# Kernel tuning notes

Hardware: AMD Instinct MI355X
Metric: run time of the kernel (lower is better)

## Reference

```python
import jax, jax.numpy as jnp
import numpy as np

N = 100000          # nodes
E = 3200000         # edges
F_IN = 128          # num_node_features
C = 32              # num_candidate_node_types


def _gcn_conv(x, src, dst, W, b, n_nodes):
    """PyG GCNConv: add self loops, symmetric deg^-1/2 normalization, then linear."""
    h = x @ W  # [N, out]
    # degree on A + I (edge weight 1), counted on target nodes
    deg = jnp.zeros((n_nodes,), h.dtype).at[dst].add(1.0) + 1.0
    dinv = jax.lax.rsqrt(deg)  # deg >= 1 so safe
    norm = dinv[src] * dinv[dst]            # [E]
    msg = h[src] * norm[:, None]            # gather + scale, [E, out]
    out = jax.ops.segment_sum(msg, dst, num_segments=n_nodes)
    out = out + h * (dinv * dinv)[:, None]  # self-loop contribution
    return out + b


def _relu6(x):
    return jnp.clip(x, 0.0, 6.0)


def setup_inputs() -> dict:
    key = jax.random.key(0)
    ks = jax.random.split(key, 16)
    def lin(k, fan_in, fan_out):
        lim = 1.0 / np.sqrt(fan_in)
        kw, kb = jax.random.split(k)
        W = jax.random.uniform(kw, (fan_in, fan_out), jnp.float32, -lim, lim)
        b = jax.random.uniform(kb, (fan_out,), jnp.float32, -lim, lim)
        return W, b
    W1, b1 = lin(ks[0], F_IN, 16)
    W2, b2 = lin(ks[1], 16, 24)
    W3, b3 = lin(ks[2], 24, 32)
    Ws1, bs1 = lin(ks[3], 32, 16)
    Ws2, bs2 = lin(ks[4], 16, C)
    We1, be1 = lin(ks[5], 32, 24)
    We2, be2 = lin(ks[6], 24, C)
    x = jax.random.normal(ks[7], (N, F_IN), jnp.float32)
    edge_index = jax.random.randint(ks[8], (2, E), 0, N, jnp.int64)
    candidate_set = jax.random.randint(ks[9], (C,), 0, C, jnp.int64)
    return dict(x=x, edge_index=edge_index, candidate_set=candidate_set,
                W1=W1, b1=b1, W2=W2, b2=b2, W3=W3, b3=b3,
                Ws1=Ws1, bs1=bs1, Ws2=Ws2, bs2=bs2,
                We1=We1, be1=be1, We2=We2, be2=be2)


def reference(x, edge_index, candidate_set,
              W1, b1, W2, b2, W3, b3,
              Ws1, bs1, Ws2, bs2, We1, be1, We2, be2):
    src, dst = edge_index[0], edge_index[1]
    h = _gcn_conv(x, src, dst, W1, b1, N)   # [N, 16] (no activation in source)
    h = _gcn_conv(h, src, dst, W2, b2, N)   # [N, 24]
    h = _gcn_conv(h, src, dst, W3, b3, N)   # [N, 32]
    # start-node head: Linear -> ReLU6 -> Linear -> Softmax, then Categorical sample
    s_logits = _relu6(h @ Ws1 + bs1) @ Ws2 + bs2         # [N, C]
    k1, k2 = jax.random.split(jax.random.key(42))
    start_node = jax.random.categorical(k1, s_logits, axis=-1)  # [N] ints in [0, C)
    # gather rows at sampled indices and append (vectorized form of the source's cat)
    combined = jnp.concatenate([h, h[start_node]], axis=0)      # [2N, 32]
    e_logits = _relu6(combined @ We1 + be1) @ We2 + be2          # [2N, C]
    end_node = jax.random.categorical(k2, e_logits, axis=-1)    # [2N]
    return start_node, end_node
```

## Files before the change

### kernel.cpp

```cpp
#include <hip/hip_runtime.h>
#include <hip/hip_bf16.h>
#include <math.h>

#define TPB 256
#define BSHIFT 8
#define BRANGE (1 << BSHIFT)
#define CHUNK 8192
#define MAXB 512

__host__ __device__ inline void tf2x32(unsigned ks0, unsigned ks1,
                                       unsigned x0, unsigned x1,
                                       unsigned& o0, unsigned& o1) {
  const unsigned ks2 = ks0 ^ ks1 ^ 0x1BD11BDAu;
  unsigned v0 = x0 + ks0, v1 = x1 + ks1;
#define TF_RND(r) { v0 += v1; v1 = (v1 << (r)) | (v1 >> (32 - (r))); v1 ^= v0; }
  TF_RND(13) TF_RND(15) TF_RND(26) TF_RND(6)
  v0 += ks1; v1 += ks2 + 1u;
  TF_RND(17) TF_RND(29) TF_RND(16) TF_RND(24)
  v0 += ks2; v1 += ks0 + 2u;
  TF_RND(13) TF_RND(15) TF_RND(26) TF_RND(6)
  v0 += ks0; v1 += ks1 + 3u;
  TF_RND(17) TF_RND(29) TF_RND(16) TF_RND(24)
  v0 += ks1; v1 += ks2 + 4u;
  TF_RND(13) TF_RND(15) TF_RND(26) TF_RND(6)
  v0 += ks2; v1 += ks0 + 5u;
#undef TF_RND
  o0 = v0; o1 = v1;
}

__device__ __forceinline__ unsigned bits32(unsigned k0, unsigned k1, unsigned idx) {
  unsigned o0, o1;
  tf2x32(k0, k1, 0u, idx, o0, o1);
  return o0 ^ o1;
}

__device__ __forceinline__ float bits_to_u(unsigned bits) {
  float f = __uint_as_float((bits >> 9) | 0x3f800000u) - 1.0f;
  return (f > 0.0f) ? f : 1.17549435e-38f;
}

__device__ __forceinline__ float gumbel_exact(unsigned k0, unsigned k1, unsigned idx) {
  float u = bits_to_u(bits32(k0, k1, idx));
  float w = (float)(-log((double)u));
  return (float)(-log((double)w));
}

__device__ __forceinline__ float gumbel_fast(unsigned k0, unsigned k1, unsigned idx) {
  float u = bits_to_u(bits32(k0, k1, idx));
  float w = -logf(u);
  return -logf(w);
}

__global__ void hist_kernel(const int* __restrict__ dst, int* __restrict__ histT,
                            int E, int nblk, int nbuckets) {
  __shared__ int hist[MAXB];
  for (int i = threadIdx.x; i < nbuckets; i += TPB) hist[i] = 0;
  __syncthreads();
  int beg = blockIdx.x * CHUNK;
  int end = min(beg + CHUNK, E);
  for (int e = beg + threadIdx.x; e < end; e += TPB)
    atomicAdd(&hist[dst[e] >> BSHIFT], 1);
  __syncthreads();
  for (int i = threadIdx.x; i < nbuckets; i += TPB)
    histT[(size_t)i * nblk + blockIdx.x] = hist[i];
}

__global__ void colscan_kernel(int* __restrict__ histT, int* __restrict__ btot, int nblk) {
  __shared__ int sh[MAXB];
  int b = blockIdx.x;
  int t = threadIdx.x;
  sh[t] = (t < nblk) ? histT[(size_t)b * nblk + t] : 0;
  __syncthreads();
  for (int ofs = 1; ofs < MAXB; ofs <<= 1) {
    int v = (t >= ofs) ? sh[t - ofs] : 0;
    __syncthreads();
    sh[t] += v;
    __syncthreads();
  }
  if (t < nblk) histT[(size_t)b * nblk + t] = (t == 0) ? 0 : sh[t - 1];
  if (t == MAXB - 1) btot[b] = sh[MAXB - 1];
}

__global__ void bucketscan_kernel(const int* __restrict__ btot, int* __restrict__ bbase,
                                  int nbuckets, int E) {
  __shared__ int sh[MAXB];
  int t = threadIdx.x;
  sh[t] = (t < nbuckets) ? btot[t] : 0;
  __syncthreads();
  for (int ofs = 1; ofs < MAXB; ofs <<= 1) {
    int v = (t >= ofs) ? sh[t - ofs] : 0;
    __syncthreads();
    sh[t] += v;
    __syncthreads();
  }
  if (t < nbuckets) bbase[t] = (t == 0) ? 0 : sh[t - 1];
  if (t == 0) bbase[nbuckets] = E;
}

__global__ void place_kernel(const int* __restrict__ src, const int* __restrict__ dst,
                             const int* __restrict__ histT, const int* __restrict__ bbase,
                             unsigned* __restrict__ packed, int E, int nblk, int nbuckets) {
  __shared__ int cur[MAXB];
  for (int i = threadIdx.x; i < nbuckets; i += TPB)
    cur[i] = histT[(size_t)i * nblk + blockIdx.x] + bbase[i];
  __syncthreads();
  int beg = blockIdx.x * CHUNK;
  int end = min(beg + CHUNK, E);
  for (int e = beg + threadIdx.x; e < end; e += TPB) {
    int s = src[e], d = dst[e];
    int b = d >> BSHIFT;
    int pos = atomicAdd(&cur[b], 1);
    packed[pos] = (unsigned)s | ((unsigned)(d & (BRANGE - 1)) << 20);
  }
}

__global__ void bucket_place_kernel(const int* __restrict__ bbase,
                                    const unsigned* __restrict__ packed,
                                    int* __restrict__ csr_src, int* __restrict__ rowptr,
                                    float* __restrict__ dinv, float* __restrict__ dinv2,
                                    int N, int nbuckets) {
  __shared__ int cnt[BRANGE];
  __shared__ int sh[BRANGE];
  __shared__ int cur[BRANGE];
  int b = blockIdx.x;
  int base = b << BSHIFT;
  int range_n = min(BRANGE, N - base);
  int t = threadIdx.x;
  cnt[t] = 0;
  __syncthreads();
  int beg = bbase[b], end = bbase[b + 1];
  for (int e = beg + t; e < end; e += TPB)
    atomicAdd(&cnt[packed[e] >> 20], 1);
  __syncthreads();
  sh[t] = cnt[t];
  __syncthreads();
  for (int ofs = 1; ofs < BRANGE; ofs <<= 1) {
    int v = (t >= ofs) ? sh[t - ofs] : 0;
    __syncthreads();
    sh[t] += v;
    __syncthreads();
  }
  int excl = (t == 0) ? 0 : sh[t - 1];
  cur[t] = beg + excl;
  if (t < range_n) {
    rowptr[base + t] = beg + excl;
    float d = (float)(cnt[t] + 1);
    float di = 1.0f / sqrtf(d);
    dinv[base + t] = di;
    dinv2[base + t] = di * di;
  }
  if (b == nbuckets - 1 && t == 0) rowptr[N] = end;
  __syncthreads();
  for (int e = beg + t; e < end; e += TPB) {
    unsigned p = packed[e];
    int dstoff = (int)(p >> 20);
    int s = (int)(p & 0xFFFFFu);
    int pos = atomicAdd(&cur[dstoff], 1);
    csr_src[pos] = s;
  }
}

template <int K, int J, int LDO, int TJ>
__global__ void matmul_tile_kernel(const float* __restrict__ A, const float* __restrict__ W,
                                   float* __restrict__ out, int N) {
  static_assert(J == TJ * 4, "each thread owns 4 outputs");
  static_assert(K % 4 == 0, "K must be multiple of 4");
  int t = blockIdx.x * blockDim.x + threadIdx.x;
  int n = t / TJ, jb = t % TJ;
  if (n >= N) return;
  const float* a = A + (size_t)n * K;
  const int j0 = jb * 4;
  double a0 = 0.0, a1 = 0.0, a2 = 0.0, a3 = 0.0;
  for (int k = 0; k < K; k += 4) {
    float4 av = *(const float4*)&a[k];
    float4 w0 = *(const float4*)&W[(k + 0) * J + j0];
    float4 w1 = *(const float4*)&W[(k + 1) * J + j0];
    float4 w2 = *(const float4*)&W[(k + 2) * J + j0];
    float4 w3 = *(const float4*)&W[(k + 3) * J + j0];
    a0 += (double)av.x * (double)w0.x; a1 += (double)av.x * (double)w0.y;
    a2 += (double)av.x * (double)w0.z; a3 += (double)av.x * (double)w0.w;
    a0 += (double)av.y * (double)w1.x; a1 += (double)av.y * (double)w1.y;
    a2 += (double)av.y * (double)w1.z; a3 += (double)av.y * (double)w1.w;
    a0 += (double)av.z * (double)w2.x; a1 += (double)av.z * (double)w2.y;
    a2 += (double)av.z * (double)w2.z; a3 += (double)av.z * (double)w2.w;
    a0 += (double)av.w * (double)w3.x; a1 += (double)av.w * (double)w3.y;
    a2 += (double)av.w * (double)w3.z; a3 += (double)av.w * (double)w3.w;
  }
  float4 o;
  o.x = (float)a0; o.y = (float)a1; o.z = (float)a2; o.w = (float)a3;
  *(float4*)&out[(size_t)n * LDO + j0] = o;
}

template <int J>
__global__ void gather_shfl_kernel(const int* __restrict__ rowptr,
                                   const int* __restrict__ csr_src,
                                   const float* __restrict__ dinv,
                                   const float* __restrict__ h,
                                   const float* __restrict__ dinv2,
                                   const float* __restrict__ b,
                                   float* __restrict__ out, int N) {
  int t = blockIdx.x * blockDim.x + threadIdx.x;
  int n = t / J, j = t % J;
  if (n >= N) return;
  int beg = rowptr[n], end = rowptr[n + 1];
  float dn = dinv[n];
  double acc = 0.0;
  for (int i = beg; i < end; i += J) {
    int m = end - i; if (m > J) m = J;
    int idx = i + j; if (idx >= end) idx = end - 1;
    int   sj = csr_src[idx];
    float wj = dinv[sj];
    int k = 0;
    for (; k + 8 <= m; k += 8) {
      int s0 = __shfl(sj, k + 0, J), s1 = __shfl(sj, k + 1, J);
      int s2 = __shfl(sj, k + 2, J), s3 = __shfl(sj, k + 3, J);
      int s4 = __shfl(sj, k + 4, J), s5 = __shfl(sj, k + 5, J);
      int s6 = __shfl(sj, k + 6, J), s7 = __shfl(sj, k + 7, J);
      float w0 = __shfl(wj, k + 0, J) * dn, w1 = __shfl(wj, k + 1, J) * dn;
      float w2 = __shfl(wj, k + 2, J) * dn, w3 = __shfl(wj, k + 3, J) * dn;
      float w4 = __shfl(wj, k + 4, J) * dn, w5 = __shfl(wj, k + 5, J) * dn;
      float w6 = __shfl(wj, k + 6, J) * dn, w7 = __shfl(wj, k + 7, J) * dn;
      float g0 = h[(size_t)s0 * J + j], g1 = h[(size_t)s1 * J + j];
      float g2 = h[(size_t)s2 * J + j], g3 = h[(size_t)s3 * J + j];
      float g4 = h[(size_t)s4 * J + j], g5 = h[(size_t)s5 * J + j];
      float g6 = h[(size_t)s6 * J + j], g7 = h[(size_t)s7 * J + j];
      acc += (double)g0 * (double)w0;
      acc += (double)g1 * (double)w1;
      acc += (double)g2 * (double)w2;
      acc += (double)g3 * (double)w3;
      acc += (double)g4 * (double)w4;
      acc += (double)g5 * (double)w5;
      acc += (double)g6 * (double)w6;
      acc += (double)g7 * (double)w7;
    }
    for (; k < m; ++k) {
      int   s = __shfl(sj, k, J);
      float w = __shfl(wj, k, J) * dn;
      acc += (double)h[(size_t)s * J + j] * (double)w;
    }
  }
  acc += (double)h[(size_t)n * J + j] * (double)dinv2[n];
  out[(size_t)n * J + j] = (float)acc + b[j];
}

template <int JA, int W, int LDH>
__global__ void gather_shfl2_kernel(const int* __restrict__ rowptr,
                                    const int* __restrict__ csr_src,
                                    const float* __restrict__ dinv,
                                    const float* __restrict__ h,
                                    const float* __restrict__ dinv2,
                                    const float* __restrict__ b,
                                    float* __restrict__ out, int N) {
  int t = blockIdx.x * blockDim.x + threadIdx.x;
  int n = t / W, j = t % W;
  if (n >= N) return;
  const int NJ = JA / 2;
  int jj = (j < NJ) ? j : (NJ - 1);
  int beg = rowptr[n], end = rowptr[n + 1];
  float dn = dinv[n];
  double acc0 = 0.0, acc1 = 0.0;
  for (int i = beg; i < end; i += W) {
    int m = end - i; if (m > W) m = W;
    int idx = i + j; if (idx >= end) idx = end - 1;
    int   sj = csr_src[idx];
    float wj = dinv[sj];
    int k = 0;
    for (; k + 8 <= m; k += 8) {
      int s0 = __shfl(sj, k + 0, W), s1 = __shfl(sj, k + 1, W);
      int s2 = __shfl(sj, k + 2, W), s3 = __shfl(sj, k + 3, W);
      int s4 = __shfl(sj, k + 4, W), s5 = __shfl(sj, k + 5, W);
      int s6 = __shfl(sj, k + 6, W), s7 = __shfl(sj, k + 7, W);
      float w0 = __shfl(wj, k + 0, W) * dn, w1 = __shfl(wj, k + 1, W) * dn;
      float w2 = __shfl(wj, k + 2, W) * dn, w3 = __shfl(wj, k + 3, W) * dn;
      float w4 = __shfl(wj, k + 4, W) * dn, w5 = __shfl(wj, k + 5, W) * dn;
      float w6 = __shfl(wj, k + 6, W) * dn, w7 = __shfl(wj, k + 7, W) * dn;
      float2 g0 = *(const float2*)&h[(size_t)s0 * LDH + 2 * jj];
      float2 g1 = *(const float2*)&h[(size_t)s1 * LDH + 2 * jj];
      float2 g2 = *(const float2*)&h[(size_t)s2 * LDH + 2 * jj];
      float2 g3 = *(const float2*)&h[(size_t)s3 * LDH + 2 * jj];
      float2 g4 = *(const float2*)&h[(size_t)s4 * LDH + 2 * jj];
      float2 g5 = *(const float2*)&h[(size_t)s5 * LDH + 2 * jj];
      float2 g6 = *(const float2*)&h[(size_t)s6 * LDH + 2 * jj];
      float2 g7 = *(const float2*)&h[(size_t)s7 * LDH + 2 * jj];
      acc0 += (double)g0.x * (double)w0; acc1 += (double)g0.y * (double)w0;
      acc0 += (double)g1.x * (double)w1; acc1 += (double)g1.y * (double)w1;
      acc0 += (double)g2.x * (double)w2; acc1 += (double)g2.y * (double)w2;
      acc0 += (double)g3.x * (double)w3; acc1 += (double)g3.y * (double)w3;
      acc0 += (double)g4.x * (double)w4; acc1 += (double)g4.y * (double)w4;
      acc0 += (double)g5.x * (double)w5; acc1 += (double)g5.y * (double)w5;
      acc0 += (double)g6.x * (double)w6; acc1 += (double)g6.y * (double)w6;
      acc0 += (double)g7.x * (double)w7; acc1 += (double)g7.y * (double)w7;
    }
    for (; k < m; ++k) {
      int   s = __shfl(sj, k, W);
      float w = __shfl(wj, k, W) * dn;
      float2 g = *(const float2*)&h[(size_t)s * LDH + 2 * jj];
      acc0 += (double)g.x * (double)w;
      acc1 += (double)g.y * (double)w;
    }
  }
  {
    float2 gs = *(const float2*)&h[(size_t)n * LDH + 2 * jj];
    double d2 = (double)dinv2[n];
    acc0 += (double)gs.x * d2;
    acc1 += (double)gs.y * d2;
  }
  if (j < NJ) {
    float2 o;
    o.x = (float)acc0 + b[2 * j];
    o.y = (float)acc1 + b[2 * j + 1];
    *(float2*)&out[(size_t)n * JA + 2 * j] = o;
  }
}

__global__ void hid_start_kernel(const float* __restrict__ h,
                                 const float* __restrict__ Ws1, const float* __restrict__ bs1,
                                 float* __restrict__ hid, int N) {
  int t = blockIdx.x * blockDim.x + threadIdx.x;
  int n = t / 4, jb = t % 4;
  if (n >= N) return;
  const float* hr = h + (size_t)n * 32;
  const int j0 = jb * 4;
  double a0 = 0.0, a1 = 0.0, a2 = 0.0, a3 = 0.0;
#pragma unroll
  for (int k = 0; k < 32; k += 4) {
    float4 av = *(const float4*)&hr[k];
    float4 w0 = *(const float4*)&Ws1[(k + 0) * 16 + j0];
    float4 w1 = *(const float4*)&Ws1[(k + 1) * 16 + j0];
    float4 w2 = *(const float4*)&Ws1[(k + 2) * 16 + j0];
    float4 w3 = *(const float4*)&Ws1[(k + 3) * 16 + j0];
    a0 += (double)av.x * (double)w0.x; a1 += (double)av.x * (double)w0.y;
    a2 += (double)av.x * (double)w0.z; a3 += (double)av.x * (double)w0.w;
    a0 += (double)av.y * (double)w1.x; a1 += (double)av.y * (double)w1.y;
    a2 += (double)av.y * (double)w1.z; a3 += (double)av.y * (double)w1.w;
    a0 += (double)av.z * (double)w2.x; a1 += (double)av.z * (double)w2.y;
    a2 += (double)av.z * (double)w2.z; a3 += (double)av.z * (double)w2.w;
    a0 += (double)av.w * (double)w3.x; a1 += (double)av.w * (double)w3.y;
    a2 += (double)av.w * (double)w3.z; a3 += (double)av.w * (double)w3.w;
  }
  float4 o;
  o.x = fminf(fmaxf((float)a0 + bs1[j0 + 0], 0.0f), 6.0f);
  o.y = fminf(fmaxf((float)a1 + bs1[j0 + 1], 0.0f), 6.0f);
  o.z = fminf(fmaxf((float)a2 + bs1[j0 + 2], 0.0f), 6.0f);
  o.w = fminf(fmaxf((float)a3 + bs1[j0 + 3], 0.0f), 6.0f);
  *(float4*)&hid[(size_t)n * 16 + j0] = o;
}

__global__ void hid_end_kernel(const float* __restrict__ h, const int* __restrict__ start,
                               const float* __restrict__ We1, const float* __restrict__ be1,
                               float* __restrict__ hid, int N) {
  int t = blockIdx.x * blockDim.x + threadIdx.x;
  int r = t / 6, jb = t % 6;
  if (r >= 2 * N) return;
  int row = (r < N) ? r : start[r - N];
  const float* hr = h + (size_t)row * 32;
  const int j0 = jb * 4;
  double a0 = 0.0, a1 = 0.0, a2 = 0.0, a3 = 0.0;
#pragma unroll
  for (int k = 0; k < 32; k += 4) {
    float4 av = *(const float4*)&hr[k];
    float4 w0 = *(const float4*)&We1[(k + 0) * 24 + j0];
    float4 w1 = *(const float4*)&We1[(k + 1) * 24 + j0];
    float4 w2 = *(const float4*)&We1[(k + 2) * 24 + j0];
    float4 w3 = *(const float4*)&We1[(k + 3) * 24 + j0];
    a0 += (double)av.x * (double)w0.x; a1 += (double)av.x * (double)w0.y;
    a2 += (double)av.x * (double)w0.z; a3 += (double)av.x * (double)w0.w;
    a0 += (double)av.y * (double)w1.x; a1 += (double)av.y * (double)w1.y;
    a2 += (double)av.y * (double)w1.z; a3 += (double)av.y * (double)w1.w;
    a0 += (double)av.z * (double)w2.x; a1 += (double)av.z * (double)w2.y;
    a2 += (double)av.z * (double)w2.z; a3 += (double)av.z * (double)w2.w;
    a0 += (double)av.w * (double)w3.x; a1 += (double)av.w * (double)w3.y;
    a2 += (double)av.w * (double)w3.z; a3 += (double)av.w * (double)w3.w;
  }
  float4 o;
  o.x = fminf(fmaxf((float)a0 + be1[j0 + 0], 0.0f), 6.0f);
  o.y = fminf(fmaxf((float)a1 + be1[j0 + 1], 0.0f), 6.0f);
  o.z = fminf(fmaxf((float)a2 + be1[j0 + 2], 0.0f), 6.0f);
  o.w = fminf(fmaxf((float)a3 + be1[j0 + 3], 0.0f), 6.0f);
  *(float4*)&hid[(size_t)r * 24 + j0] = o;
}

template <int K>
__global__ void pick_kernel(const float* __restrict__ hid,
                            const float* __restrict__ W2, const float* __restrict__ b2,
                            int* __restrict__ outw, int R, unsigned k0, unsigned k1) {
  int t = blockIdx.x * blockDim.x + threadIdx.x;
  int r = t >> 5;
  int c = t & 31;
  if (r >= R) return;
  const float* hr = hid + (size_t)r * K;

  float af = 0.0f;
#pragma unroll
  for (int k = 0; k < K; ++k) af = fmaf(hr[k], W2[k * 32 + c], af);
  float zf = af + b2[c] + gumbel_fast(k0, k1, (unsigned)(r * 32 + c));

  float m1 = zf; int i1 = c; float m2 = -INFINITY;
#pragma unroll
  for (int m = 16; m >= 1; m >>= 1) {
    float om1 = __shfl_xor(m1, m, 32);
    int   oi1 = __shfl_xor(i1, m, 32);
    float om2 = __shfl_xor(m2, m, 32);
    if (om1 > m1 || (om1 == m1 && oi1 < i1)) {
      m2 = fmaxf(m1, om2);
      m1 = om1; i1 = oi1;
    } else {
      m2 = fmaxf(m2, om1);
    }
  }

  if (m1 - m2 >= 1e-3f) {
    if (c == 0) outw[r] = i1;
    return;
  }

  double a = 0.0;
#pragma unroll
  for (int k = 0; k < K; ++k) a += (double)hr[k] * (double)W2[k * 32 + c];
  float logit = (float)a + b2[c];
  float z = logit + gumbel_exact(k0, k1, (unsigned)(r * 32 + c));
  int best = c;
#pragma unroll
  for (int m = 16; m >= 1; m >>= 1) {
    float oz = __shfl_xor(z, m, 32);
    int   ob = __shfl_xor(best, m, 32);
    if (oz > z || (oz == z && ob < best)) { z = oz; best = ob; }
  }
  if (c == 0) outw[r] = best;
}

extern "C" void kernel_launch(void* const* d_in, const int* in_sizes, int n_in,
                              void* d_out, int out_size, void* d_ws, size_t ws_size,
                              hipStream_t stream) {
  const float* x   = (const float*)d_in[0];
  const int*   ei  = (const int*)d_in[1];
  const float* W1  = (const float*)d_in[3];
  const float* b1  = (const float*)d_in[4];
  const float* W2  = (const float*)d_in[5];
  const float* b2  = (const float*)d_in[6];
  const float* W3  = (const float*)d_in[7];
  const float* b3  = (const float*)d_in[8];
  const float* Ws1 = (const float*)d_in[9];
  const float* bs1 = (const float*)d_in[10];
  const float* Ws2 = (const float*)d_in[11];
  const float* bs2 = (const float*)d_in[12];
  const float* We1 = (const float*)d_in[13];
  const float* be1 = (const float*)d_in[14];
  const float* We2 = (const float*)d_in[15];
  const float* be2 = (const float*)d_in[16];

  const int N = in_sizes[0] / 128;
  const int E = in_sizes[1] / 2;
  const int* srcv = ei;
  const int* dstv = ei + E;
  const int nbuckets = (N + BRANGE - 1) >> BSHIFT;
  const int nblk = (E + CHUNK - 1) / CHUNK;

  char* ws = (char*)d_ws;
  size_t off = 0;
  float*    hA      = (float*)(ws + off);    off += (size_t)N * 32 * 4;
  float*    hB      = (float*)(ws + off);    off += (size_t)N * 32 * 4;
  int*      csr_src = (int*)(ws + off);      off += (size_t)E * 4;
  unsigned* packed  = (unsigned*)(ws + off); off += (size_t)E * 4;
  float*    dinv    = (float*)(ws + off);    off += (size_t)N * 4;
  float*    dinv2   = (float*)(ws + off);    off += (size_t)N * 4;
  int*      rowptr  = (int*)(ws + off);      off += (size_t)(N + 1) * 4;
  int*      histT   = (int*)(ws + off);      off += (size_t)nbuckets * nblk * 4;
  int*      btot    = (int*)(ws + off);      off += (size_t)MAXB * 4;
  int*      bbase   = (int*)(ws + off);      off += (size_t)(MAXB + 1) * 4;
  float* hid_start = hA;
  float* hid_end   = (float*)csr_src;

  unsigned k1a, k1b, k2a, k2b;
  tf2x32(0u, 42u, 0u, 0u, k1a, k1b);
  tf2x32(0u, 42u, 0u, 1u, k2a, k2b);

  hist_kernel<<<nblk, TPB, 0, stream>>>(dstv, histT, E, nblk, nbuckets);
  colscan_kernel<<<nbuckets, MAXB, 0, stream>>>(histT, btot, nblk);
  bucketscan_kernel<<<1, MAXB, 0, stream>>>(btot, bbase, nbuckets, E);
  place_kernel<<<nblk, TPB, 0, stream>>>(srcv, dstv, histT, bbase, packed, E, nblk, nbuckets);
  bucket_place_kernel<<<nbuckets, TPB, 0, stream>>>(bbase, packed, csr_src, rowptr,
                                                    dinv, dinv2, N, nbuckets);

  matmul_tile_kernel<128, 16, 16, 4><<<((size_t)N * 4 + TPB - 1) / TPB, TPB, 0, stream>>>(x, W1, hA, N);
  gather_shfl_kernel<16><<<((size_t)N * 16 + TPB - 1) / TPB, TPB, 0, stream>>>(
      rowptr, csr_src, dinv, hA, dinv2, b1, hB, N);

  matmul_tile_kernel<16, 24, 32, 6><<<((size_t)N * 6 + TPB - 1) / TPB, TPB, 0, stream>>>(hB, W2, hA, N);
  gather_shfl2_kernel<24, 16, 32><<<((size_t)N * 16 + TPB - 1) / TPB, TPB, 0, stream>>>(
      rowptr, csr_src, dinv, hA, dinv2, b2, hB, N);

  matmul_tile_kernel<24, 32, 32, 8><<<((size_t)N * 8 + TPB - 1) / TPB, TPB, 0, stream>>>(hB, W3, hA, N);
  gather_shfl2_kernel<32, 16, 32><<<((size_t)N * 16 + TPB - 1) / TPB, TPB, 0, stream>>>(
      rowptr, csr_src, dinv, hA, dinv2, b3, hB, N);

  int* outI = (int*)d_out;

  hid_start_kernel<<<((size_t)N * 4 + TPB - 1) / TPB, TPB, 0, stream>>>(hB, Ws1, bs1, hid_start, N);
  pick_kernel<16><<<((size_t)N * 32 + TPB - 1) / TPB, TPB, 0, stream>>>(
      hid_start, Ws2, bs2, outI, N, k1a, k1b);

  hid_end_kernel<<<((size_t)2 * N * 6 + TPB - 1) / TPB, TPB, 0, stream>>>(hB, outI, We1, be1, hid_end, N);
  pick_kernel<24><<<((size_t)2 * N * 32 + TPB - 1) / TPB, TPB, 0, stream>>>(
      hid_end, We2, be2, outI + N, 2 * N, k2a, k2b);
}
```

Before: 515.5 us.

## Fuse head MLP layers into pick kernel and overlap first matmul with histogram

```diff
diff --git a/kernel.cpp b/kernel.cpp
--- a/kernel.cpp
+++ b/kernel.cpp
@@ -51,18 +51,47 @@
   return -logf(w);
 }
 
-__global__ void hist_kernel(const int* __restrict__ dst, int* __restrict__ histT,
-                            int E, int nblk, int nbuckets) {
+__global__ void hist_mm_kernel(const int* __restrict__ dst, int* __restrict__ histT,
+                               int E, int nblk, int nbuckets,
+                               const float* __restrict__ A, const float* __restrict__ W,
+                               float* __restrict__ out, int N) {
   __shared__ int hist[MAXB];
-  for (int i = threadIdx.x; i < nbuckets; i += TPB) hist[i] = 0;
-  __syncthreads();
-  int beg = blockIdx.x * CHUNK;
-  int end = min(beg + CHUNK, E);
-  for (int e = beg + threadIdx.x; e < end; e += TPB)
-    atomicAdd(&hist[dst[e] >> BSHIFT], 1);
-  __syncthreads();
-  for (int i = threadIdx.x; i < nbuckets; i += TPB)
-    histT[(size_t)i * nblk + blockIdx.x] = hist[i];
+  if ((int)blockIdx.x < nblk) {
+    for (int i = threadIdx.x; i < nbuckets; i += TPB) hist[i] = 0;
+    __syncthreads();
+    int beg = blockIdx.x * CHUNK;
+    int end = min(beg + CHUNK, E);
+    for (int e = beg + threadIdx.x; e < end; e += TPB)
+      atomicAdd(&hist[dst[e] >> BSHIFT], 1);
+    __syncthreads();
+    for (int i = threadIdx.x; i < nbuckets; i += TPB)
+      histT[(size_t)i * nblk + blockIdx.x] = hist[i];
+  } else {
+    int t = ((int)blockIdx.x - nblk) * TPB + threadIdx.x;
+    int n = t / 4, jb = t % 4;
+    if (n >= N) return;
+    const float* a = A + (size_t)n * 128;
+    const int j0 = jb * 4;
+    double a0 = 0.0, a1 = 0.0, a2 = 0.0, a3 = 0.0;
+    for (int k = 0; k < 128; k += 4) {
+      float4 av = *(const float4*)&a[k];
+      float4 w0 = *(const float4*)&W[(k + 0) * 16 + j0];
+      float4 w1 = *(const float4*)&W[(k + 1) * 16 + j0];
+      float4 w2 = *(const float4*)&W[(k + 2) * 16 + j0];
+      float4 w3 = *(const float4*)&W[(k + 3) * 16 + j0];
+      a0 += (double)av.x * (double)w0.x; a1 += (double)av.x * (double)w0.y;
+      a2 += (double)av.x * (double)w0.z; a3 += (double)av.x * (double)w0.w;
+      a0 += (double)av.y * (double)w1.x; a1 += (double)av.y * (double)w1.y;
+      a2 += (double)av.y * (double)w1.z; a3 += (double)av.y * (double)w1.w;
+      a0 += (double)av.z * (double)w2.x; a1 += (double)av.z * (double)w2.y;
+      a2 += (double)av.z * (double)w2.z; a3 += (double)av.z * (double)w2.w;
+      a0 += (double)av.w * (double)w3.x; a1 += (double)av.w * (double)w3.y;
+      a2 += (double)av.w * (double)w3.z; a3 += (double)av.w * (double)w3.w;
+    }
+    float4 o;
+    o.x = (float)a0; o.y = (float)a1; o.z = (float)a2; o.w = (float)a3;
+    *(float4*)&out[(size_t)n * 16 + j0] = o;
+  }
 }
 
 __global__ void colscan_kernel(int* __restrict__ histT, int* __restrict__ btot, int nblk) {
@@ -313,87 +342,30 @@
   }
 }
 
-__global__ void hid_start_kernel(const float* __restrict__ h,
-                                 const float* __restrict__ Ws1, const float* __restrict__ bs1,
-                                 float* __restrict__ hid, int N) {
-  int t = blockIdx.x * blockDim.x + threadIdx.x;
-  int n = t / 4, jb = t % 4;
-  if (n >= N) return;
-  const float* hr = h + (size_t)n * 32;
-  const int j0 = jb * 4;
-  double a0 = 0.0, a1 = 0.0, a2 = 0.0, a3 = 0.0;
-#pragma unroll
-  for (int k = 0; k < 32; k += 4) {
-    float4 av = *(const float4*)&hr[k];
-    float4 w0 = *(const float4*)&Ws1[(k + 0) * 16 + j0];
-    float4 w1 = *(const float4*)&Ws1[(k + 1) * 16 + j0];
-    float4 w2 = *(const float4*)&Ws1[(k + 2) * 16 + j0];
-    float4 w3 = *(const float4*)&Ws1[(k + 3) * 16 + j0];
-    a0 += (double)av.x * (double)w0.x; a1 += (double)av.x * (double)w0.y;
-    a2 += (double)av.x * (double)w0.z; a3 += (double)av.x * (double)w0.w;
-    a0 += (double)av.y * (double)w1.x; a1 += (double)av.y * (double)w1.y;
-    a2 += (double)av.y * (double)w1.z; a3 += (double)av.y * (double)w1.w;
-    a0 += (double)av.z * (double)w2.x; a1 += (double)av.z * (double)w2.y;
-    a2 += (double)av.z * (double)w2.z; a3 += (double)av.z * (double)w2.w;
-    a0 += (double)av.w * (double)w3.x; a1 += (double)av.w * (double)w3.y;
-    a2 += (double)av.w * (double)w3.z; a3 += (double)av.w * (double)w3.w;
-  }
-  float4 o;
-  o.x = fminf(fmaxf((float)a0 + bs1[j0 + 0], 0.0f), 6.0f);
-  o.y = fminf(fmaxf((float)a1 + bs1[j0 + 1], 0.0f), 6.0f);
-  o.z = fminf(fmaxf((float)a2 + bs1[j0 + 2], 0.0f), 6.0f);
-  o.w = fminf(fmaxf((float)a3 + bs1[j0 + 3], 0.0f), 6.0f);
-  *(float4*)&hid[(size_t)n * 16 + j0] = o;
-}
-
-__global__ void hid_end_kernel(const float* __restrict__ h, const int* __restrict__ start,
-                               const float* __restrict__ We1, const float* __restrict__ be1,
-                               float* __restrict__ hid, int N) {
-  int t = blockIdx.x * blockDim.x + threadIdx.x;
-  int r = t / 6, jb = t % 6;
-  if (r >= 2 * N) return;
-  int row = (r < N) ? r : start[r - N];
-  const float* hr = h + (size_t)row * 32;
-  const int j0 = jb * 4;
-  double a0 = 0.0, a1 = 0.0, a2 = 0.0, a3 = 0.0;
-#pragma unroll
-  for (int k = 0; k < 32; k += 4) {
-    float4 av = *(const float4*)&hr[k];
-    float4 w0 = *(const float4*)&We1[(k + 0) * 24 + j0];
-    float4 w1 = *(const float4*)&We1[(k + 1) * 24 + j0];
-    float4 w2 = *(const float4*)&We1[(k + 2) * 24 + j0];
-    float4 w3 = *(const float4*)&We1[(k + 3) * 24 + j0];
-    a0 += (double)av.x * (double)w0.x; a1 += (double)av.x * (double)w0.y;
-    a2 += (double)av.x * (double)w0.z; a3 += (double)av.x * (double)w0.w;
-    a0 += (double)av.y * (double)w1.x; a1 += (double)av.y * (double)w1.y;
-    a2 += (double)av.y * (double)w1.z; a3 += (double)av.y * (double)w1.w;
-    a0 += (double)av.z * (double)w2.x; a1 += (double)av.z * (double)w2.y;
-    a2 += (double)av.z * (double)w2.z; a3 += (double)av.z * (double)w2.w;
-    a0 += (double)av.w * (double)w3.x; a1 += (double)av.w * (double)w3.y;
-    a2 += (double)av.w * (double)w3.z; a3 += (double)av.w * (double)w3.w;
-  }
-  float4 o;
-  o.x = fminf(fmaxf((float)a0 + be1[j0 + 0], 0.0f), 6.0f);
-  o.y = fminf(fmaxf((float)a1 + be1[j0 + 1], 0.0f), 6.0f);
-  o.z = fminf(fmaxf((float)a2 + be1[j0 + 2], 0.0f), 6.0f);
-  o.w = fminf(fmaxf((float)a3 + be1[j0 + 3], 0.0f), 6.0f);
-  *(float4*)&hid[(size_t)r * 24 + j0] = o;
-}
-
-template <int K>
-__global__ void pick_kernel(const float* __restrict__ hid,
-                            const float* __restrict__ W2, const float* __restrict__ b2,
+template <int KH>
+__global__ void head_kernel(const float* __restrict__ h,
+                            const int* __restrict__ start, int NN,
+                            const float* __restrict__ W1h, const float* __restrict__ b1h,
+                            const float* __restrict__ W2h, const float* __restrict__ b2h,
                             int* __restrict__ outw, int R, unsigned k0, unsigned k1) {
   int t = blockIdx.x * blockDim.x + threadIdx.x;
   int r = t >> 5;
   int c = t & 31;
   if (r >= R) return;
-  const float* hr = hid + (size_t)r * K;
+  int row = r;
+  if (start != nullptr && r >= NN) row = start[r - NN];
+  const float* hr = h + (size_t)row * 32;
+
+  int cc = (c < KH) ? c : (KH - 1);
+  double ah = 0.0;
+#pragma unroll
+  for (int k = 0; k < 32; ++k) ah += (double)hr[k] * (double)W1h[k * KH + cc];
+  float hid = fminf(fmaxf((float)ah + b1h[cc], 0.0f), 6.0f);
 
   float af = 0.0f;
 #pragma unroll
-  for (int k = 0; k < K; ++k) af = fmaf(hr[k], W2[k * 32 + c], af);
-  float zf = af + b2[c] + gumbel_fast(k0, k1, (unsigned)(r * 32 + c));
+  for (int k = 0; k < KH; ++k) af = fmaf(__shfl(hid, k, 32), W2h[k * 32 + c], af);
+  float zf = af + b2h[c] + gumbel_fast(k0, k1, (unsigned)(r * 32 + c));
 
   float m1 = zf; int i1 = c; float m2 = -INFINITY;
 #pragma unroll
@@ -416,8 +388,8 @@
 
   double a = 0.0;
 #pragma unroll
-  for (int k = 0; k < K; ++k) a += (double)hr[k] * (double)W2[k * 32 + c];
-  float logit = (float)a + b2[c];
+  for (int k = 0; k < KH; ++k) a += (double)__shfl(hid, k, 32) * (double)W2h[k * 32 + c];
+  float logit = (float)a + b2h[c];
   float z = logit + gumbel_exact(k0, k1, (unsigned)(r * 32 + c));
   int best = c;
 #pragma unroll
@@ -468,21 +440,20 @@
   int*      histT   = (int*)(ws + off);      off += (size_t)nbuckets * nblk * 4;
   int*      btot    = (int*)(ws + off);      off += (size_t)MAXB * 4;
   int*      bbase   = (int*)(ws + off);      off += (size_t)(MAXB + 1) * 4;
-  float* hid_start = hA;
-  float* hid_end   = (float*)csr_src;
 
   unsigned k1a, k1b, k2a, k2b;
   tf2x32(0u, 42u, 0u, 0u, k1a, k1b);
   tf2x32(0u, 42u, 0u, 1u, k2a, k2b);
 
-  hist_kernel<<<nblk, TPB, 0, stream>>>(dstv, histT, E, nblk, nbuckets);
+  const int mmblk = (int)(((size_t)N * 4 + TPB - 1) / TPB);
+  hist_mm_kernel<<<nblk + mmblk, TPB, 0, stream>>>(dstv, histT, E, nblk, nbuckets,
+                                                   x, W1, hA, N);
   colscan_kernel<<<nbuckets, MAXB, 0, stream>>>(histT, btot, nblk);
   bucketscan_kernel<<<1, MAXB, 0, stream>>>(btot, bbase, nbuckets, E);
   place_kernel<<<nblk, TPB, 0, stream>>>(srcv, dstv, histT, bbase, packed, E, nblk, nbuckets);
   bucket_place_kernel<<<nbuckets, TPB, 0, stream>>>(bbase, packed, csr_src, rowptr,
                                                     dinv, dinv2, N, nbuckets);
 
-  matmul_tile_kernel<128, 16, 16, 4><<<((size_t)N * 4 + TPB - 1) / TPB, TPB, 0, stream>>>(x, W1, hA, N);
   gather_shfl_kernel<16><<<((size_t)N * 16 + TPB - 1) / TPB, TPB, 0, stream>>>(
       rowptr, csr_src, dinv, hA, dinv2, b1, hB, N);
 
@@ -496,11 +467,9 @@
 
   int* outI = (int*)d_out;
 
-  hid_start_kernel<<<((size_t)N * 4 + TPB - 1) / TPB, TPB, 0, stream>>>(hB, Ws1, bs1, hid_start, N);
-  pick_kernel<16><<<((size_t)N * 32 + TPB - 1) / TPB, TPB, 0, stream>>>(
-      hid_start, Ws2, bs2, outI, N, k1a, k1b);
-
-  hid_end_kernel<<<((size_t)2 * N * 6 + TPB - 1) / TPB, TPB, 0, stream>>>(hB, outI, We1, be1, hid_end, N);
-  pick_kernel<24><<<((size_t)2 * N * 32 + TPB - 1) / TPB, TPB, 0, stream>>>(
-      hid_end, We2, be2, outI + N, 2 * N, k2a, k2b);
-}
+  head_kernel<16><<<((size_t)N * 32 + TPB - 1) / TPB, TPB, 0, stream>>>(
+      hB, nullptr, N, Ws1, bs1, Ws2, bs2, outI, N, k1a, k1b);
+
+  head_kernel<24><<<((size_t)2 * N * 32 + TPB - 1) / TPB, TPB, 0, stream>>>(
+      hB, outI, N, We1, be1, We2, be2, outI + N, 2 * N, k2a, k2b);
+}
```

Result: slower. 528.9 us (+2.6%).

## Fuse small matmuls into gather epilogues and merge first matmul with histogram

Applied to the files above, without the earlier changes.

```diff
diff --git a/kernel.cpp b/kernel.cpp
--- a/kernel.cpp
+++ b/kernel.cpp
@@ -51,18 +51,47 @@
   return -logf(w);
 }
 
-__global__ void hist_kernel(const int* __restrict__ dst, int* __restrict__ histT,
-                            int E, int nblk, int nbuckets) {
+__global__ void hist_mm_kernel(const int* __restrict__ dst, int* __restrict__ histT,
+                               int E, int nblk, int nbuckets,
+                               const float* __restrict__ A, const float* __restrict__ W,
+                               float* __restrict__ out, int N) {
   __shared__ int hist[MAXB];
-  for (int i = threadIdx.x; i < nbuckets; i += TPB) hist[i] = 0;
-  __syncthreads();
-  int beg = blockIdx.x * CHUNK;
-  int end = min(beg + CHUNK, E);
-  for (int e = beg + threadIdx.x; e < end; e += TPB)
-    atomicAdd(&hist[dst[e] >> BSHIFT], 1);
-  __syncthreads();
-  for (int i = threadIdx.x; i < nbuckets; i += TPB)
-    histT[(size_t)i * nblk + blockIdx.x] = hist[i];
+  if ((int)blockIdx.x < nblk) {
+    for (int i = threadIdx.x; i < nbuckets; i += TPB) hist[i] = 0;
+    __syncthreads();
+    int beg = blockIdx.x * CHUNK;
+    int end = min(beg + CHUNK, E);
+    for (int e = beg + threadIdx.x; e < end; e += TPB)
+      atomicAdd(&hist[dst[e] >> BSHIFT], 1);
+    __syncthreads();
+    for (int i = threadIdx.x; i < nbuckets; i += TPB)
+      histT[(size_t)i * nblk + blockIdx.x] = hist[i];
+  } else {
+    int t = ((int)blockIdx.x - nblk) * TPB + threadIdx.x;
+    int n = t / 4, jb = t % 4;
+    if (n >= N) return;
+    const float* a = A + (size_t)n * 128;
+    const int j0 = jb * 4;
+    double a0 = 0.0, a1 = 0.0, a2 = 0.0, a3 = 0.0;
+    for (int k = 0; k < 128; k += 4) {
+      float4 av = *(const float4*)&a[k];
+      float4 w0 = *(const float4*)&W[(k + 0) * 16 + j0];
+      float4 w1 = *(const float4*)&W[(k + 1) * 16 + j0];
+      float4 w2 = *(const float4*)&W[(k + 2) * 16 + j0];
+      float4 w3 = *(const float4*)&W[(k + 3) * 16 + j0];
+      a0 += (double)av.x * (double)w0.x; a1 += (double)av.x * (double)w0.y;
+      a2 += (double)av.x * (double)w0.z; a3 += (double)av.x * (double)w0.w;
+      a0 += (double)av.y * (double)w1.x; a1 += (double)av.y * (double)w1.y;
+      a2 += (double)av.y * (double)w1.z; a3 += (double)av.y * (double)w1.w;
+      a0 += (double)av.z * (double)w2.x; a1 += (double)av.z * (double)w2.y;
+      a2 += (double)av.z * (double)w2.z; a3 += (double)av.z * (double)w2.w;
+      a0 += (double)av.w * (double)w3.x; a1 += (double)av.w * (double)w3.y;
+      a2 += (double)av.w * (double)w3.z; a3 += (double)av.w * (double)w3.w;
+    }
+    float4 o;
+    o.x = (float)a0; o.y = (float)a1; o.z = (float)a2; o.w = (float)a3;
+    *(float4*)&out[(size_t)n * 16 + j0] = o;
+  }
 }
 
 __global__ void colscan_kernel(int* __restrict__ histT, int* __restrict__ btot, int nblk) {
@@ -160,45 +189,15 @@
   }
 }
 
-template <int K, int J, int LDO, int TJ>
-__global__ void matmul_tile_kernel(const float* __restrict__ A, const float* __restrict__ W,
-                                   float* __restrict__ out, int N) {
-  static_assert(J == TJ * 4, "each thread owns 4 outputs");
-  static_assert(K % 4 == 0, "K must be multiple of 4");
-  int t = blockIdx.x * blockDim.x + threadIdx.x;
-  int n = t / TJ, jb = t % TJ;
-  if (n >= N) return;
-  const float* a = A + (size_t)n * K;
-  const int j0 = jb * 4;
-  double a0 = 0.0, a1 = 0.0, a2 = 0.0, a3 = 0.0;
-  for (int k = 0; k < K; k += 4) {
-    float4 av = *(const float4*)&a[k];
-    float4 w0 = *(const float4*)&W[(k + 0) * J + j0];
-    float4 w1 = *(const float4*)&W[(k + 1) * J + j0];
-    float4 w2 = *(const float4*)&W[(k + 2) * J + j0];
-    float4 w3 = *(const float4*)&W[(k + 3) * J + j0];
-    a0 += (double)av.x * (double)w0.x; a1 += (double)av.x * (double)w0.y;
-    a2 += (double)av.x * (double)w0.z; a3 += (double)av.x * (double)w0.w;
-    a0 += (double)av.y * (double)w1.x; a1 += (double)av.y * (double)w1.y;
-    a2 += (double)av.y * (double)w1.z; a3 += (double)av.y * (double)w1.w;
-    a0 += (double)av.z * (double)w2.x; a1 += (double)av.z * (double)w2.y;
-    a2 += (double)av.z * (double)w2.z; a3 += (double)av.z * (double)w2.w;
-    a0 += (double)av.w * (double)w3.x; a1 += (double)av.w * (double)w3.y;
-    a2 += (double)av.w * (double)w3.z; a3 += (double)av.w * (double)w3.w;
-  }
-  float4 o;
-  o.x = (float)a0; o.y = (float)a1; o.z = (float)a2; o.w = (float)a3;
-  *(float4*)&out[(size_t)n * LDO + j0] = o;
-}
-
-template <int J>
-__global__ void gather_shfl_kernel(const int* __restrict__ rowptr,
+__global__ void gather1_mm2_kernel(const int* __restrict__ rowptr,
                                    const int* __restrict__ csr_src,
                                    const float* __restrict__ dinv,
                                    const float* __restrict__ h,
                                    const float* __restrict__ dinv2,
                                    const float* __restrict__ b,
+                                   const float* __restrict__ W2,
                                    float* __restrict__ out, int N) {
+  constexpr int J = 16;
   int t = blockIdx.x * blockDim.x + threadIdx.x;
   int n = t / J, j = t % J;
   if (n >= N) return;
@@ -240,7 +239,101 @@
     }
   }
   acc += (double)h[(size_t)n * J + j] * (double)dinv2[n];
-  out[(size_t)n * J + j] = (float)acc + b[j];
+  float hv = (float)acc + b[j];
+
+  int j2 = (j < 12) ? j : 11;
+  double m0 = 0.0, m1 = 0.0;
+#pragma unroll
+  for (int k = 0; k < 16; ++k) {
+    float hk = __shfl(hv, k, J);
+    m0 += (double)hk * (double)W2[k * 24 + 2 * j2];
+    m1 += (double)hk * (double)W2[k * 24 + 2 * j2 + 1];
+  }
+  if (j < 12) {
+    float2 o;
+    o.x = (float)m0; o.y = (float)m1;
+    *(float2*)&out[(size_t)n * 32 + 2 * j] = o;
+  }
+}
+
+__global__ void gather2_mm3_kernel(const int* __restrict__ rowptr,
+                                   const int* __restrict__ csr_src,
+                                   const float* __restrict__ dinv,
+                                   const float* __restrict__ h,
+                                   const float* __restrict__ dinv2,
+                                   const float* __restrict__ b,
+                                   const float* __restrict__ W3,
+                                   float* __restrict__ out, int N) {
+  constexpr int W = 16, LDH = 32;
+  int t = blockIdx.x * blockDim.x + threadIdx.x;
+  int n = t / W, j = t % W;
+  if (n >= N) return;
+  int jj = (j < 12) ? j : 11;
+  int beg = rowptr[n], end = rowptr[n + 1];
+  float dn = dinv[n];
+  double acc0 = 0.0, acc1 = 0.0;
+  for (int i = beg; i < end; i += W) {
+    int m = end - i; if (m > W) m = W;
+    int idx = i + j; if (idx >= end) idx = end - 1;
+    int   sj = csr_src[idx];
+    float wj = dinv[sj];
+    int k = 0;
+    for (; k + 8 <= m; k += 8) {
+      int s0 = __shfl(sj, k + 0, W), s1 = __shfl(sj, k + 1, W);
+      int s2 = __shfl(sj, k + 2, W), s3 = __shfl(sj, k + 3, W);
+      int s4 = __shfl(sj, k + 4, W), s5 = __shfl(sj, k + 5, W);
+      int s6 = __shfl(sj, k + 6, W), s7 = __shfl(sj, k + 7, W);
+      float w0 = __shfl(wj, k + 0, W) * dn, w1 = __shfl(wj, k + 1, W) * dn;
+      float w2 = __shfl(wj, k + 2, W) * dn, w3 = __shfl(wj, k + 3, W) * dn;
+      float w4 = __shfl(wj, k + 4, W) * dn, w5 = __shfl(wj, k + 5, W) * dn;
+      float w6 = __shfl(wj, k + 6, W) * dn, w7 = __shfl(wj, k + 7, W) * dn;
+      float2 g0 = *(const float2*)&h[(size_t)s0 * LDH + 2 * jj];
+      float2 g1 = *(const float2*)&h[(size_t)s1 * LDH + 2 * jj];
+      float2 g2 = *(const float2*)&h[(size_t)s2 * LDH + 2 * jj];
+      float2 g3 = *(const float2*)&h[(size_t)s3 * LDH + 2 * jj];
+      float2 g4 = *(const float2*)&h[(size_t)s4 * LDH + 2 * jj];
+      float2 g5 = *(const float2*)&h[(size_t)s5 * LDH + 2 * jj];
+      float2 g6 = *(const float2*)&h[(size_t)s6 * LDH + 2 * jj];
+      float2 g7 = *(const float2*)&h[(size_t)s7 * LDH + 2 * jj];
+      acc0 += (double)g0.x * (double)w0; acc1 += (double)g0.y * (double)w0;
+      acc0 += (double)g1.x * (double)w1; acc1 += (double)g1.y * (double)w1;
+      acc0 += (double)g2.x * (double)w2; acc1 += (double)g2.y * (double)w2;
+      acc0 += (double)g3.x * (double)w3; acc1 += (double)g3.y * (double)w3;
+      acc0 += (double)g4.x * (double)w4; acc1 += (double)g4.y * (double)w4;
+      acc0 += (double)g5.x * (double)w5; acc1 += (double)g5.y * (double)w5;
+      acc0 += (double)g6.x * (double)w6; acc1 += (double)g6.y * (double)w6;
+      acc0 += (double)g7.x * (double)w7; acc1 += (double)g7.y * (double)w7;
+    }
+    for (; k < m; ++k) {
+      int   s = __shfl(sj, k, W);
+      float w = __shfl(wj, k, W) * dn;
+      float2 g = *(const float2*)&h[(size_t)s * LDH + 2 * jj];
+      acc0 += (double)g.x * (double)w;
+      acc1 += (double)g.y * (double)w;
+    }
+  }
+  {
+    float2 gs = *(const float2*)&h[(size_t)n * LDH + 2 * jj];
+    double d2 = (double)dinv2[n];
+    acc0 += (double)gs.x * d2;
+    acc1 += (double)gs.y * d2;
+  }
+  float h0 = (float)acc0 + b[2 * jj];
+  float h1 = (float)acc1 + b[2 * jj + 1];
+
+  double m0 = 0.0, m1 = 0.0;
+#pragma unroll
+  for (int k = 0; k < 12; ++k) {
+    float e0 = __shfl(h0, k, W);
+    float e1 = __shfl(h1, k, W);
+    m0 += (double)e0 * (double)W3[(2 * k) * 32 + 2 * j];
+    m0 += (double)e1 * (double)W3[(2 * k + 1) * 32 + 2 * j];
+    m1 += (double)e0 * (double)W3[(2 * k) * 32 + 2 * j + 1];
+    m1 += (double)e1 * (double)W3[(2 * k + 1) * 32 + 2 * j + 1];
+  }
+  float2 o;
+  o.x = (float)m0; o.y = (float)m1;
+  *(float2*)&out[(size_t)n * 32 + 2 * j] = o;
 }
 
 template <int JA, int W, int LDH>
@@ -475,22 +568,21 @@
   tf2x32(0u, 42u, 0u, 0u, k1a, k1b);
   tf2x32(0u, 42u, 0u, 1u, k2a, k2b);
 
-  hist_kernel<<<nblk, TPB, 0, stream>>>(dstv, histT, E, nblk, nbuckets);
+  const int mmblk = (int)(((size_t)N * 4 + TPB - 1) / TPB);
+  hist_mm_kernel<<<nblk + mmblk, TPB, 0, stream>>>(dstv, histT, E, nblk, nbuckets,
+                                                   x, W1, hA, N);
   colscan_kernel<<<nbuckets, MAXB, 0, stream>>>(histT, btot, nblk);
   bucketscan_kernel<<<1, MAXB, 0, stream>>>(btot, bbase, nbuckets, E);
   place_kernel<<<nblk, TPB, 0, stream>>>(srcv, dstv, histT, bbase, packed, E, nblk, nbuckets);
   bucket_place_kernel<<<nbuckets, TPB, 0, stream>>>(bbase, packed, csr_src, rowptr,
                                                     dinv, dinv2, N, nbuckets);
 
-  matmul_tile_kernel<128, 16, 16, 4><<<((size_t)N * 4 + TPB - 1) / TPB, TPB, 0, stream>>>(x, W1, hA, N);
-  gather_shfl_kernel<16><<<((size_t)N * 16 + TPB - 1) / TPB, TPB, 0, stream>>>(
-      rowptr, csr_src, dinv, hA, dinv2, b1, hB, N);
-
-  matmul_tile_kernel<16, 24, 32, 6><<<((size_t)N * 6 + TPB - 1) / TPB, TPB, 0, stream>>>(hB, W2, hA, N);
-  gather_shfl2_kernel<24, 16, 32><<<((size_t)N * 16 + TPB - 1) / TPB, TPB, 0, stream>>>(
-      rowptr, csr_src, dinv, hA, dinv2, b2, hB, N);
-
-  matmul_tile_kernel<24, 32, 32, 8><<<((size_t)N * 8 + TPB - 1) / TPB, TPB, 0, stream>>>(hB, W3, hA, N);
+  gather1_mm2_kernel<<<((size_t)N * 16 + TPB - 1) / TPB, TPB, 0, stream>>>(
+      rowptr, csr_src, dinv, hA, dinv2, b1, W2, hB, N);
+
+  gather2_mm3_kernel<<<((size_t)N * 16 + TPB - 1) / TPB, TPB, 0, stream>>>(
+      rowptr, csr_src, dinv, hB, dinv2, b2, W3, hA, N);
+
   gather_shfl2_kernel<32, 16, 32><<<((size_t)N * 16 + TPB - 1) / TPB, TPB, 0, stream>>>(
       rowptr, csr_src, dinv, hA, dinv2, b3, hB, N);
 
```

Result: no change. 509.6 us (-1.1%).

## Fuse first matmul into histogram launch and second matmul into layer-1 gather

Applied to the files above, without the earlier changes.

```diff
diff --git a/kernel.cpp b/kernel.cpp
--- a/kernel.cpp
+++ b/kernel.cpp
@@ -51,18 +51,47 @@
   return -logf(w);
 }
 
-__global__ void hist_kernel(const int* __restrict__ dst, int* __restrict__ histT,
-                            int E, int nblk, int nbuckets) {
+__global__ void hist_mm_kernel(const int* __restrict__ dst, int* __restrict__ histT,
+                               int E, int nblk, int nbuckets,
+                               const float* __restrict__ A, const float* __restrict__ W,
+                               float* __restrict__ out, int N) {
   __shared__ int hist[MAXB];
-  for (int i = threadIdx.x; i < nbuckets; i += TPB) hist[i] = 0;
-  __syncthreads();
-  int beg = blockIdx.x * CHUNK;
-  int end = min(beg + CHUNK, E);
-  for (int e = beg + threadIdx.x; e < end; e += TPB)
-    atomicAdd(&hist[dst[e] >> BSHIFT], 1);
-  __syncthreads();
-  for (int i = threadIdx.x; i < nbuckets; i += TPB)
-    histT[(size_t)i * nblk + blockIdx.x] = hist[i];
+  if ((int)blockIdx.x < nblk) {
+    for (int i = threadIdx.x; i < nbuckets; i += TPB) hist[i] = 0;
+    __syncthreads();
+    int beg = blockIdx.x * CHUNK;
+    int end = min(beg + CHUNK, E);
+    for (int e = beg + threadIdx.x; e < end; e += TPB)
+      atomicAdd(&hist[dst[e] >> BSHIFT], 1);
+    __syncthreads();
+    for (int i = threadIdx.x; i < nbuckets; i += TPB)
+      histT[(size_t)i * nblk + blockIdx.x] = hist[i];
+  } else {
+    int t = ((int)blockIdx.x - nblk) * TPB + threadIdx.x;
+    int n = t / 4, jb = t % 4;
+    if (n >= N) return;
+    const float* a = A + (size_t)n * 128;
+    const int j0 = jb * 4;
+    double a0 = 0.0, a1 = 0.0, a2 = 0.0, a3 = 0.0;
+    for (int k = 0; k < 128; k += 4) {
+      float4 av = *(const float4*)&a[k];
+      float4 w0 = *(const float4*)&W[(k + 0) * 16 + j0];
+      float4 w1 = *(const float4*)&W[(k + 1) * 16 + j0];
+      float4 w2 = *(const float4*)&W[(k + 2) * 16 + j0];
+      float4 w3 = *(const float4*)&W[(k + 3) * 16 + j0];
+      a0 += (double)av.x * (double)w0.x; a1 += (double)av.x * (double)w0.y;
+      a2 += (double)av.x * (double)w0.z; a3 += (double)av.x * (double)w0.w;
+      a0 += (double)av.y * (double)w1.x; a1 += (double)av.y * (double)w1.y;
+      a2 += (double)av.y * (double)w1.z; a3 += (double)av.y * (double)w1.w;
+      a0 += (double)av.z * (double)w2.x; a1 += (double)av.z * (double)w2.y;
+      a2 += (double)av.z * (double)w2.z; a3 += (double)av.z * (double)w2.w;
+      a0 += (double)av.w * (double)w3.x; a1 += (double)av.w * (double)w3.y;
+      a2 += (double)av.w * (double)w3.z; a3 += (double)av.w * (double)w3.w;
+    }
+    float4 o;
+    o.x = (float)a0; o.y = (float)a1; o.z = (float)a2; o.w = (float)a3;
+    *(float4*)&out[(size_t)n * 16 + j0] = o;
+  }
 }
 
 __global__ void colscan_kernel(int* __restrict__ histT, int* __restrict__ btot, int nblk) {
@@ -191,14 +220,15 @@
   *(float4*)&out[(size_t)n * LDO + j0] = o;
 }
 
-template <int J>
-__global__ void gather_shfl_kernel(const int* __restrict__ rowptr,
+__global__ void gather1_mm2_kernel(const int* __restrict__ rowptr,
                                    const int* __restrict__ csr_src,
                                    const float* __restrict__ dinv,
                                    const float* __restrict__ h,
                                    const float* __restrict__ dinv2,
                                    const float* __restrict__ b,
+                                   const float* __restrict__ W2,
                                    float* __restrict__ out, int N) {
+  constexpr int J = 16;
   int t = blockIdx.x * blockDim.x + threadIdx.x;
   int n = t / J, j = t % J;
   if (n >= N) return;
@@ -240,7 +270,22 @@
     }
   }
   acc += (double)h[(size_t)n * J + j] * (double)dinv2[n];
-  out[(size_t)n * J + j] = (float)acc + b[j];
+  float hv = (float)acc + b[j];
+
+  int j2 = (j < 12) ? j : 11;
+  double m0 = 0.0, m1 = 0.0;
+#pragma unroll
+  for (int k = 0; k < 16; ++k) {
+    float hk = __shfl(hv, k, J);
+    float2 wv = *(const float2*)&W2[k * 24 + 2 * j2];
+    m0 += (double)hk * (double)wv.x;
+    m1 += (double)hk * (double)wv.y;
+  }
+  if (j < 12) {
+    float2 o;
+    o.x = (float)m0; o.y = (float)m1;
+    *(float2*)&out[(size_t)n * 32 + 2 * j] = o;
+  }
 }
 
 template <int JA, int W, int LDH>
@@ -384,6 +429,7 @@
 __global__ void pick_kernel(const float* __restrict__ hid,
                             const float* __restrict__ W2, const float* __restrict__ b2,
                             int* __restrict__ outw, int R, unsigned k0, unsigned k1) {
+  static_assert(K % 4 == 0, "K must be multiple of 4");
   int t = blockIdx.x * blockDim.x + threadIdx.x;
   int r = t >> 5;
   int c = t & 31;
@@ -392,7 +438,13 @@
 
   float af = 0.0f;
 #pragma unroll
-  for (int k = 0; k < K; ++k) af = fmaf(hr[k], W2[k * 32 + c], af);
+  for (int q = 0; q < K; q += 4) {
+    float4 v = *(const float4*)&hr[q];
+    af = fmaf(v.x, W2[(q + 0) * 32 + c], af);
+    af = fmaf(v.y, W2[(q + 1) * 32 + c], af);
+    af = fmaf(v.z, W2[(q + 2) * 32 + c], af);
+    af = fmaf(v.w, W2[(q + 3) * 32 + c], af);
+  }
   float zf = af + b2[c] + gumbel_fast(k0, k1, (unsigned)(r * 32 + c));
 
   float m1 = zf; int i1 = c; float m2 = -INFINITY;
@@ -416,7 +468,13 @@
 
   double a = 0.0;
 #pragma unroll
-  for (int k = 0; k < K; ++k) a += (double)hr[k] * (double)W2[k * 32 + c];
+  for (int q = 0; q < K; q += 4) {
+    float4 v = *(const float4*)&hr[q];
+    a += (double)v.x * (double)W2[(q + 0) * 32 + c];
+    a += (double)v.y * (double)W2[(q + 1) * 32 + c];
+    a += (double)v.z * (double)W2[(q + 2) * 32 + c];
+    a += (double)v.w * (double)W2[(q + 3) * 32 + c];
+  }
   float logit = (float)a + b2[c];
   float z = logit + gumbel_exact(k0, k1, (unsigned)(r * 32 + c));
   int best = c;
@@ -468,39 +526,40 @@
   int*      histT   = (int*)(ws + off);      off += (size_t)nbuckets * nblk * 4;
   int*      btot    = (int*)(ws + off);      off += (size_t)MAXB * 4;
   int*      bbase   = (int*)(ws + off);      off += (size_t)(MAXB + 1) * 4;
-  float* hid_start = hA;
+  float* hid_start = hB;
   float* hid_end   = (float*)csr_src;
 
   unsigned k1a, k1b, k2a, k2b;
   tf2x32(0u, 42u, 0u, 0u, k1a, k1b);
   tf2x32(0u, 42u, 0u, 1u, k2a, k2b);
 
-  hist_kernel<<<nblk, TPB, 0, stream>>>(dstv, histT, E, nblk, nbuckets);
+  const int mmblk = (int)(((size_t)N * 4 + TPB - 1) / TPB);
+  hist_mm_kernel<<<nblk + mmblk, TPB, 0, stream>>>(dstv, histT, E, nblk, nbuckets,
+                                                   x, W1, hA, N);
   colscan_kernel<<<nbuckets, MAXB, 0, stream>>>(histT, btot, nblk);
   bucketscan_kernel<<<1, MAXB, 0, stream>>>(btot, bbase, nbuckets, E);
   place_kernel<<<nblk, TPB, 0, stream>>>(srcv, dstv, histT, bbase, packed, E, nblk, nbuckets);
   bucket_place_kernel<<<nbuckets, TPB, 0, stream>>>(bbase, packed, csr_src, rowptr,
                                                     dinv, dinv2, N, nbuckets);
 
-  matmul_tile_kernel<128, 16, 16, 4><<<((size_t)N * 4 + TPB - 1) / TPB, TPB, 0, stream>>>(x, W1, hA, N);
-  gather_shfl_kernel<16><<<((size_t)N * 16 + TPB - 1) / TPB, TPB, 0, stream>>>(
-      rowptr, csr_src, dinv, hA, dinv2, b1, hB, N);
-
-  matmul_tile_kernel<16, 24, 32, 6><<<((size_t)N * 6 + TPB - 1) / TPB, TPB, 0, stream>>>(hB, W2, hA, N);
+  gather1_mm2_kernel<<<((size_t)N * 16 + TPB - 1) / TPB, TPB, 0, stream>>>(
+      rowptr, csr_src, dinv, hA, dinv2, b1, W2, hB, N);
+
   gather_shfl2_kernel<24, 16, 32><<<((size_t)N * 16 + TPB - 1) / TPB, TPB, 0, stream>>>(
-      rowptr, csr_src, dinv, hA, dinv2, b2, hB, N);
-
-  matmul_tile_kernel<24, 32, 32, 8><<<((size_t)N * 8 + TPB - 1) / TPB, TPB, 0, stream>>>(hB, W3, hA, N);
+      rowptr, csr_src, dinv, hB, dinv2, b2, hA, N);
+
+  matmul_tile_kernel<24, 32, 32, 8><<<((size_t)N * 8 + TPB - 1) / TPB, TPB, 0, stream>>>(hA, W3, hB, N);
+
   gather_shfl2_kernel<32, 16, 32><<<((size_t)N * 16 + TPB - 1) / TPB, TPB, 0, stream>>>(
-      rowptr, csr_src, dinv, hA, dinv2, b3, hB, N);
+      rowptr, csr_src, dinv, hB, dinv2, b3, hA, N);
 
   int* outI = (int*)d_out;
 
-  hid_start_kernel<<<((size_t)N * 4 + TPB - 1) / TPB, TPB, 0, stream>>>(hB, Ws1, bs1, hid_start, N);
+  hid_start_kernel<<<((size_t)N * 4 + TPB - 1) / TPB, TPB, 0, stream>>>(hA, Ws1, bs1, hid_start, N);
   pick_kernel<16><<<((size_t)N * 32 + TPB - 1) / TPB, TPB, 0, stream>>>(
       hid_start, Ws2, bs2, outI, N, k1a, k1b);
 
-  hid_end_kernel<<<((size_t)2 * N * 6 + TPB - 1) / TPB, TPB, 0, stream>>>(hB, outI, We1, be1, hid_end, N);
+  hid_end_kernel<<<((size_t)2 * N * 6 + TPB - 1) / TPB, TPB, 0, stream>>>(hA, outI, We1, be1, hid_end, N);
   pick_kernel<24><<<((size_t)2 * N * 32 + TPB - 1) / TPB, TPB, 0, stream>>>(
       hid_end, We2, be2, outI + N, 2 * N, k2a, k2b);
 }
```

Measured after the change: 519.2 us. No clear change (+0.7%).
